# Kernel optimization log

Measured on AMD Instinct MI355X. Metric: run time of the kernel, lower is better.

Reference implementation:

```python
import jax, jax.numpy as jnp
import numpy as np

VOCAB, EMBD, H1, H2, OUT = 100000, 128, 256, 128, 1
EPS = 1e-12

def _layernorm(x, g, b):
    mu = jnp.mean(x, axis=-1, keepdims=True)
    var = jnp.mean(jnp.square(x - mu), axis=-1, keepdims=True)
    return (x - mu) * jax.lax.rsqrt(var + EPS) * g + b

def setup_inputs() -> dict:
    key = jax.random.key(0)
    ks = jax.random.split(key, 10)
    B, S = 4096, 50
    return {
        "entity_ids": jax.random.randint(ks[0], (B, S), 0, VOCAB),
        "entity_length": jax.random.randint(ks[1], (B,), 0, S + 1),
        "emb_table": jax.random.normal(ks[2], (VOCAB, EMBD), jnp.float32),
        "ln1_g": jnp.ones((EMBD,), jnp.float32),
        "ln1_b": jnp.zeros((EMBD,), jnp.float32),
        "w1": jax.random.normal(ks[3], (EMBD, H1), jnp.float32) * (1.0 / np.sqrt(EMBD)),
        "b1": jnp.zeros((H1,), jnp.float32),
        "w2": jax.random.normal(ks[4], (H1, H2), jnp.float32) * (1.0 / np.sqrt(H1)),
        "b2": jnp.zeros((H2,), jnp.float32),
        "ln2_g": jnp.ones((H2,), jnp.float32),
        "ln2_b": jnp.zeros((H2,), jnp.float32),
        "fc_w": jax.random.normal(ks[5], (H2, OUT), jnp.float32) * (1.0 / np.sqrt(H2)),
        "fc_b": jnp.zeros((OUT,), jnp.float32),
    }

def reference(entity_ids, entity_length, emb_table, ln1_g, ln1_b, w1, b1, w2, b2, ln2_g, ln2_b, fc_w, fc_b):
    # embed: [B, S, EMBD]
    x = emb_table[entity_ids]
    x = _layernorm(x, ln1_g, ln1_b)
    # MLP (dropout is identity in eval); torch GELU default is exact erf form
    x = jax.nn.gelu(x @ w1 + b1, approximate=False) @ w2 + b2  # [B, S, H2]
    # ragged max-pool over first length positions (length 0 treated as 1)
    lengths = jnp.maximum(entity_length, 1)  # [B]
    S = x.shape[1]
    mask = jnp.arange(S)[None, :] < lengths[:, None]  # [B, S]
    x = jnp.max(jnp.where(mask[:, :, None], x, -jnp.inf), axis=1)  # [B, H2]
    x = _layernorm(x, ln2_g, ln2_b)
    return (x @ fc_w + fc_b).squeeze(-1)  # [B]
```

## Files before the change

### kernel.cpp

```cpp
#include <hip/hip_runtime.h>
#include <hip/hip_bf16.h>
#include <math.h>

typedef __attribute__((ext_vector_type(8))) short short8;
typedef __attribute__((ext_vector_type(4))) float f32x4;

#define EMBD 128
#define H1 256
#define H2 128
#define SLEN 50

__device__ __forceinline__ short f2bf(float f) {
    __hip_bfloat16 h = __float2bfloat16(f);
    return *reinterpret_cast<short*>(&h);
}

__device__ __forceinline__ float gelu_exact(float h) {
    float ah = fabsf(h);
    float d  = fmaf(0.23163845f, ah, 1.0f);
    float t;
    asm("v_rcp_f32 %0, %1" : "=v"(t) : "v"(d));
    float p = fmaf(1.061405429f, t, -1.453152027f);
    p = fmaf(p, t, 1.421413741f);
    p = fmaf(p, t, -0.284496736f);
    p = fmaf(p, t, 0.254829592f);
    p = p * t;
    float e;
    float x2 = h * h * -0.72134752f;
    asm("v_exp_f32 %0, %1" : "=v"(e) : "v"(x2));
    float er = fmaf(-p, e, 1.0f);
    return fmaf(0.5f * ah, er, 0.5f * h);
}

#define BARRIER_LDS() asm volatile("s_waitcnt lgkmcnt(0)\n\ts_barrier" ::: "memory")

__global__ __launch_bounds__(256) void prep_weights(
    const float* __restrict__ w1, const float* __restrict__ w2,
    short8* __restrict__ ws)
{
    int f = blockIdx.x * 256 + threadIdx.x;
    short8 v;
    if (f < 4096) {
        int lane = f & 63;
        int nt = (f >> 6) & 3, kt = (f >> 8) & 3, w = (f >> 10) & 3;
        int col = w * 64 + nt * 16 + (lane & 15);
        int kb  = kt * 32 + (lane >> 4) * 8;
        #pragma unroll
        for (int i = 0; i < 8; ++i) v[i] = f2bf(w1[(size_t)(kb + i) * H1 + col]);
        ws[f] = v;
    } else {
        int f2 = f - 4096;
        int lane = f2 & 63;
        int nt = (f2 >> 6) & 1, kt = (f2 >> 7) & 7, w = (f2 >> 10) & 3;
        int col = w * 32 + nt * 16 + (lane & 15);
        int kb  = kt * 32 + (lane >> 4) * 8;
        #pragma unroll
        for (int i = 0; i < 8; ++i) v[i] = f2bf(w2[(size_t)(kb + i) * H2 + col]);
        ws[4096 + f2] = v;
    }
}

__global__ __launch_bounds__(256) void entity_encoder_kernel(
    const int* __restrict__ ids, const int* __restrict__ lens,
    const float* __restrict__ emb, const float* __restrict__ ln1g,
    const float* __restrict__ ln1b, const float* __restrict__ b1,
    const float* __restrict__ b2, const float* __restrict__ ln2g,
    const float* __restrict__ ln2b, const float* __restrict__ fcw,
    const float* __restrict__ fcb, const short8* __restrict__ wfrag,
    float* __restrict__ out)
{
    const int tid = threadIdx.x;
    const int w  = tid >> 6;
    const int l  = tid & 63;
    const int ln = l & 15;
    const int lg = l >> 4;

    __shared__ __align__(16) short x_lds[16][EMBD + 8];
    __shared__ __align__(16) short h1_lds[16][H1 + 8];
    __shared__ float pool_lds[H2];

    short8 w1f[4][4];
    #pragma unroll
    for (int kt = 0; kt < 4; ++kt)
      #pragma unroll
      for (int nt = 0; nt < 4; ++nt)
        w1f[kt][nt] = wfrag[((w * 4 + kt) * 4 + nt) * 64 + l];
    short8 w2f[8][2];
    #pragma unroll
    for (int kt = 0; kt < 8; ++kt)
      #pragma unroll
      for (int nt = 0; nt < 2; ++nt)
        w2f[kt][nt] = wfrag[4096 + ((w * 8 + kt) * 2 + nt) * 64 + l];

    float g1r[8], b1r[8];
    #pragma unroll
    for (int i = 0; i < 8; ++i) { g1r[i] = ln1g[ln * 8 + i]; b1r[i] = ln1b[ln * 8 + i]; }
    float b1v[4];
    #pragma unroll
    for (int nt = 0; nt < 4; ++nt) b1v[nt] = b1[w * 64 + nt * 16 + ln];
    float b2v[2];
    #pragma unroll
    for (int nt = 0; nt < 2; ++nt) b2v[nt] = b2[w * 32 + nt * 16 + ln];
    float g2a = ln2g[l], g2c = ln2g[l + 64];
    float b2a = ln2b[l], b2c = ln2b[l + 64];
    float fwa = fcw[l],  fwc = fcw[l + 64];
    float fcb0 = fcb[0];

    const int r = blockIdx.x;
    int T = lens[r]; T = T < 1 ? 1 : (T > SLEN ? SLEN : T);
    const int ntiles = (T + 15) >> 4;
    float pool0 = -INFINITY, pool1 = -INFINITY;

    const int tok = w * 4 + lg;

    float4 pa0, pa1; bool va;
    {
        int t = tok; va = (t < T);
        if (va) {
            int id = ids[r * SLEN + t];
            const float4* src = (const float4*)(emb + (size_t)id * EMBD + ln * 8);
            pa0 = src[0]; pa1 = src[1];
        }
    }

    for (int mt = 0; mt < ntiles; ++mt) {
        short8 xo;
        if (va) {
            float v[8] = {pa0.x, pa0.y, pa0.z, pa0.w, pa1.x, pa1.y, pa1.z, pa1.w};
            float s = 0.f, ss = 0.f;
            #pragma unroll
            for (int i = 0; i < 8; ++i) { s += v[i]; ss += v[i] * v[i]; }
            #pragma unroll
            for (int m = 1; m < 16; m <<= 1) {
                s  += __shfl_xor(s,  m, 64);
                ss += __shfl_xor(ss, m, 64);
            }
            float mu  = s * (1.f / 128.f);
            float var = ss * (1.f / 128.f) - mu * mu;
            float rs  = rsqrtf(var + 1e-12f);
            #pragma unroll
            for (int i = 0; i < 8; ++i)
                xo[i] = f2bf((v[i] - mu) * rs * g1r[i] + b1r[i]);
        } else {
            #pragma unroll
            for (int i = 0; i < 8; ++i) xo[i] = 0;
        }
        *(short8*)&x_lds[tok][ln * 8] = xo;

        float4 pb0, pb1; bool vb = false;
        {
            int tn = (mt + 1) * 16 + tok;
            if (mt + 1 < ntiles && tn < T) {
                vb = true;
                int id = ids[r * SLEN + tn];
                const float4* src = (const float4*)(emb + (size_t)id * EMBD + ln * 8);
                pb0 = src[0]; pb1 = src[1];
            }
        }

        BARRIER_LDS();

        f32x4 acc[4] = {{0,0,0,0},{0,0,0,0},{0,0,0,0},{0,0,0,0}};
        #pragma unroll
        for (int kt = 0; kt < 4; ++kt) {
            short8 a = *(const short8*)&x_lds[ln][kt * 32 + lg * 8];
            #pragma unroll
            for (int nt = 0; nt < 4; ++nt)
                acc[nt] = __builtin_amdgcn_mfma_f32_16x16x32_bf16(a, w1f[kt][nt], acc[nt], 0, 0, 0);
        }
        #pragma unroll
        for (int nt = 0; nt < 4; ++nt) {
            int col = w * 64 + nt * 16 + ln;
            #pragma unroll
            for (int g2 = 0; g2 < 4; ++g2) {
                int row = lg * 4 + g2;
                float h = acc[nt][g2] + b1v[nt];
                h1_lds[row][col] = f2bf(gelu_exact(h));
            }
        }

        BARRIER_LDS();

        f32x4 acc2[2] = {{0,0,0,0},{0,0,0,0}};
        #pragma unroll
        for (int kt = 0; kt < 8; ++kt) {
            short8 a = *(const short8*)&h1_lds[ln][kt * 32 + lg * 8];
            #pragma unroll
            for (int nt = 0; nt < 2; ++nt)
                acc2[nt] = __builtin_amdgcn_mfma_f32_16x16x32_bf16(a, w2f[kt][nt], acc2[nt], 0, 0, 0);
        }
        {
            float tm0 = -INFINITY, tm1 = -INFINITY;
            #pragma unroll
            for (int g2 = 0; g2 < 4; ++g2) {
                int trow = lg * 4 + g2;
                bool valid = (mt * 16 + trow) < T;
                float h0  = acc2[0][g2] + b2v[0];
                float h1v = acc2[1][g2] + b2v[1];
                if (valid) { tm0 = fmaxf(tm0, h0); tm1 = fmaxf(tm1, h1v); }
            }
            tm0 = fmaxf(tm0, __shfl_xor(tm0, 16, 64));
            tm0 = fmaxf(tm0, __shfl_xor(tm0, 32, 64));
            tm1 = fmaxf(tm1, __shfl_xor(tm1, 16, 64));
            tm1 = fmaxf(tm1, __shfl_xor(tm1, 32, 64));
            pool0 = fmaxf(pool0, tm0);
            pool1 = fmaxf(pool1, tm1);
        }

        if (vb) { pa0 = pb0; pa1 = pb1; }
        va = vb;
    }

    if (l < 16) {
        pool_lds[w * 32 + ln]      = pool0;
        pool_lds[w * 32 + 16 + ln] = pool1;
    }
    __syncthreads();

    float v0 = pool_lds[l], v1 = pool_lds[l + 64];
    float s = v0 + v1, ss = v0 * v0 + v1 * v1;
    #pragma unroll
    for (int m = 1; m < 64; m <<= 1) {
        s  += __shfl_xor(s,  m, 64);
        ss += __shfl_xor(ss, m, 64);
    }
    float mu  = s * (1.f / 128.f);
    float var = ss * (1.f / 128.f) - mu * mu;
    float rs  = rsqrtf(var + 1e-12f);
    float n0 = (v0 - mu) * rs * g2a + b2a;
    float n1 = (v1 - mu) * rs * g2c + b2c;
    float dot = n0 * fwa + n1 * fwc;
    #pragma unroll
    for (int m = 1; m < 64; m <<= 1) dot += __shfl_xor(dot, m, 64);
    if (tid == 0) out[r] = dot + fcb0;
}

extern "C" void kernel_launch(void* const* d_in, const int* in_sizes, int n_in,
                              void* d_out, int out_size, void* d_ws, size_t ws_size,
                              hipStream_t stream) {
    const int*   ids  = (const int*)d_in[0];
    const int*   lens = (const int*)d_in[1];
    const float* emb  = (const float*)d_in[2];
    const float* ln1g = (const float*)d_in[3];
    const float* ln1b = (const float*)d_in[4];
    const float* w1   = (const float*)d_in[5];
    const float* b1   = (const float*)d_in[6];
    const float* w2   = (const float*)d_in[7];
    const float* b2   = (const float*)d_in[8];
    const float* ln2g = (const float*)d_in[9];
    const float* ln2b = (const float*)d_in[10];
    const float* fcw  = (const float*)d_in[11];
    const float* fcb  = (const float*)d_in[12];
    float* out = (float*)d_out;
    short8* ws = (short8*)d_ws;

    hipLaunchKernelGGL(prep_weights, dim3(32), dim3(256), 0, stream, w1, w2, ws);

    int nblocks = out_size;
    hipLaunchKernelGGL(entity_encoder_kernel, dim3(nblocks), dim3(256), 0, stream,
                       ids, lens, emb, ln1g, ln1b, b1, b2, ln2g, ln2b, fcw, fcb,
                       ws, out);
}
```

Measured before the change: 74.53 us.

## Process four batch rows per block to amortize weight fragment loads

Each block now handles NR=4 batch rows, strided by grid size, instead of one. The per-block setup of loading W1/W2 MFMA fragments and LayerNorm parameters into registers is paid once per four rows. The embedding prefetch now carries across row boundaries. The cost is a quarter as many blocks (1024 on a 4096 batch), which cuts parallelism and latency hiding. Ragged lengths also make per-block work less even.

```diff
diff --git a/kernel.cpp b/kernel.cpp
--- a/kernel.cpp
+++ b/kernel.cpp
@@ -9,6 +9,7 @@
 #define H1 256
 #define H2 128
 #define SLEN 50
+#define NR 4
 
 __device__ __forceinline__ short f2bf(float f) {
     __hip_bfloat16 h = __float2bfloat16(f);
@@ -106,133 +107,150 @@
     float fwa = fcw[l],  fwc = fcw[l + 64];
     float fcb0 = fcb[0];
 
-    const int r = blockIdx.x;
-    int T = lens[r]; T = T < 1 ? 1 : (T > SLEN ? SLEN : T);
-    const int ntiles = (T + 15) >> 4;
-    float pool0 = -INFINITY, pool1 = -INFINITY;
-
+    const int stride = gridDim.x;
     const int tok = w * 4 + lg;
+
+    int rows[NR], Ts[NR];
+    #pragma unroll
+    for (int i = 0; i < NR; ++i) {
+        rows[i] = blockIdx.x + i * stride;
+        int T = lens[rows[i]];
+        Ts[i] = T < 1 ? 1 : (T > SLEN ? SLEN : T);
+    }
 
     float4 pa0, pa1; bool va;
     {
-        int t = tok; va = (t < T);
+        va = (tok < Ts[0]);
         if (va) {
-            int id = ids[r * SLEN + t];
+            int id = ids[rows[0] * SLEN + tok];
             const float4* src = (const float4*)(emb + (size_t)id * EMBD + ln * 8);
             pa0 = src[0]; pa1 = src[1];
         }
     }
 
-    for (int mt = 0; mt < ntiles; ++mt) {
-        short8 xo;
-        if (va) {
-            float v[8] = {pa0.x, pa0.y, pa0.z, pa0.w, pa1.x, pa1.y, pa1.z, pa1.w};
-            float s = 0.f, ss = 0.f;
+    for (int i = 0; i < NR; ++i) {
+        const int r = rows[i];
+        const int T = Ts[i];
+        const int ntiles = (T + 15) >> 4;
+        float pool0 = -INFINITY, pool1 = -INFINITY;
+
+        for (int mt = 0; mt < ntiles; ++mt) {
+            short8 xo;
+            if (va) {
+                float v[8] = {pa0.x, pa0.y, pa0.z, pa0.w, pa1.x, pa1.y, pa1.z, pa1.w};
+                float s = 0.f, ss = 0.f;
+                #pragma unroll
+                for (int k = 0; k < 8; ++k) { s += v[k]; ss += v[k] * v[k]; }
+                #pragma unroll
+                for (int m = 1; m < 16; m <<= 1) {
+                    s  += __shfl_xor(s,  m, 64);
+                    ss += __shfl_xor(ss, m, 64);
+                }
+                float mu  = s * (1.f / 128.f);
+                float var = ss * (1.f / 128.f) - mu * mu;
+                float rs  = rsqrtf(var + 1e-12f);
+                #pragma unroll
+                for (int k = 0; k < 8; ++k)
+                    xo[k] = f2bf((v[k] - mu) * rs * g1r[k] + b1r[k]);
+            } else {
+                #pragma unroll
+                for (int k = 0; k < 8; ++k) xo[k] = 0;
+            }
+            *(short8*)&x_lds[tok][ln * 8] = xo;
+
+            float4 pb0, pb1; bool vb = false;
+            {
+                int ni = i, nmt = mt + 1;
+                if (nmt >= ntiles) { ni = i + 1; nmt = 0; }
+                if (ni < NR) {
+                    int tn = nmt * 16 + tok;
+                    if (tn < Ts[ni]) {
+                        vb = true;
+                        int id = ids[rows[ni] * SLEN + tn];
+                        const float4* src = (const float4*)(emb + (size_t)id * EMBD + ln * 8);
+                        pb0 = src[0]; pb1 = src[1];
+                    }
+                }
+            }
+
+            BARRIER_LDS();
+
+            f32x4 acc[4] = {{0,0,0,0},{0,0,0,0},{0,0,0,0},{0,0,0,0}};
             #pragma unroll
-            for (int i = 0; i < 8; ++i) { s += v[i]; ss += v[i] * v[i]; }
+            for (int kt = 0; kt < 4; ++kt) {
+                short8 a = *(const short8*)&x_lds[ln][kt * 32 + lg * 8];
+                #pragma unroll
+                for (int nt = 0; nt < 4; ++nt)
+                    acc[nt] = __builtin_amdgcn_mfma_f32_16x16x32_bf16(a, w1f[kt][nt], acc[nt], 0, 0, 0);
+            }
             #pragma unroll
-            for (int m = 1; m < 16; m <<= 1) {
-                s  += __shfl_xor(s,  m, 64);
-                ss += __shfl_xor(ss, m, 64);
-            }
-            float mu  = s * (1.f / 128.f);
-            float var = ss * (1.f / 128.f) - mu * mu;
-            float rs  = rsqrtf(var + 1e-12f);
+            for (int nt = 0; nt < 4; ++nt) {
+                int col = w * 64 + nt * 16 + ln;
+                #pragma unroll
+                for (int g2 = 0; g2 < 4; ++g2) {
+                    int row = lg * 4 + g2;
+                    float h = acc[nt][g2] + b1v[nt];
+                    h1_lds[row][col] = f2bf(gelu_exact(h));
+                }
+            }
+
+            BARRIER_LDS();
+
+            f32x4 acc2[2] = {{0,0,0,0},{0,0,0,0}};
             #pragma unroll
-            for (int i = 0; i < 8; ++i)
-                xo[i] = f2bf((v[i] - mu) * rs * g1r[i] + b1r[i]);
-        } else {
-            #pragma unroll
-            for (int i = 0; i < 8; ++i) xo[i] = 0;
-        }
-        *(short8*)&x_lds[tok][ln * 8] = xo;
-
-        float4 pb0, pb1; bool vb = false;
-        {
-            int tn = (mt + 1) * 16 + tok;
-            if (mt + 1 < ntiles && tn < T) {
-                vb = true;
-                int id = ids[r * SLEN + tn];
-                const float4* src = (const float4*)(emb + (size_t)id * EMBD + ln * 8);
-                pb0 = src[0]; pb1 = src[1];
-            }
-        }
-
+            for (int kt = 0; kt < 8; ++kt) {
+                short8 a = *(const short8*)&h1_lds[ln][kt * 32 + lg * 8];
+                #pragma unroll
+                for (int nt = 0; nt < 2; ++nt)
+                    acc2[nt] = __builtin_amdgcn_mfma_f32_16x16x32_bf16(a, w2f[kt][nt], acc2[nt], 0, 0, 0);
+            }
+            {
+                float tm0 = -INFINITY, tm1 = -INFINITY;
+                #pragma unroll
+                for (int g2 = 0; g2 < 4; ++g2) {
+                    int trow = lg * 4 + g2;
+                    bool valid = (mt * 16 + trow) < T;
+                    float h0  = acc2[0][g2] + b2v[0];
+                    float h1v = acc2[1][g2] + b2v[1];
+                    if (valid) { tm0 = fmaxf(tm0, h0); tm1 = fmaxf(tm1, h1v); }
+                }
+                tm0 = fmaxf(tm0, __shfl_xor(tm0, 16, 64));
+                tm0 = fmaxf(tm0, __shfl_xor(tm0, 32, 64));
+                tm1 = fmaxf(tm1, __shfl_xor(tm1, 16, 64));
+                tm1 = fmaxf(tm1, __shfl_xor(tm1, 32, 64));
+                pool0 = fmaxf(pool0, tm0);
+                pool1 = fmaxf(pool1, tm1);
+            }
+
+            if (vb) { pa0 = pb0; pa1 = pb1; }
+            va = vb;
+        }
+
+        if (l < 16) {
+            pool_lds[w * 32 + ln]      = pool0;
+            pool_lds[w * 32 + 16 + ln] = pool1;
+        }
         BARRIER_LDS();
 
-        f32x4 acc[4] = {{0,0,0,0},{0,0,0,0},{0,0,0,0},{0,0,0,0}};
-        #pragma unroll
-        for (int kt = 0; kt < 4; ++kt) {
-            short8 a = *(const short8*)&x_lds[ln][kt * 32 + lg * 8];
-            #pragma unroll
-            for (int nt = 0; nt < 4; ++nt)
-                acc[nt] = __builtin_amdgcn_mfma_f32_16x16x32_bf16(a, w1f[kt][nt], acc[nt], 0, 0, 0);
-        }
-        #pragma unroll
-        for (int nt = 0; nt < 4; ++nt) {
-            int col = w * 64 + nt * 16 + ln;
-            #pragma unroll
-            for (int g2 = 0; g2 < 4; ++g2) {
-                int row = lg * 4 + g2;
-                float h = acc[nt][g2] + b1v[nt];
-                h1_lds[row][col] = f2bf(gelu_exact(h));
-            }
-        }
+        float v0 = pool_lds[l], v1 = pool_lds[l + 64];
+        float s = v0 + v1, ss = v0 * v0 + v1 * v1;
+        #pragma unroll
+        for (int m = 1; m < 64; m <<= 1) {
+            s  += __shfl_xor(s,  m, 64);
+            ss += __shfl_xor(ss, m, 64);
+        }
+        float mu  = s * (1.f / 128.f);
+        float var = ss * (1.f / 128.f) - mu * mu;
+        float rs  = rsqrtf(var + 1e-12f);
+        float n0 = (v0 - mu) * rs * g2a + b2a;
+        float n1 = (v1 - mu) * rs * g2c + b2c;
+        float dot = n0 * fwa + n1 * fwc;
+        #pragma unroll
+        for (int m = 1; m < 64; m <<= 1) dot += __shfl_xor(dot, m, 64);
+        if (tid == 0) out[r] = dot + fcb0;
 
         BARRIER_LDS();
-
-        f32x4 acc2[2] = {{0,0,0,0},{0,0,0,0}};
-        #pragma unroll
-        for (int kt = 0; kt < 8; ++kt) {
-            short8 a = *(const short8*)&h1_lds[ln][kt * 32 + lg * 8];
-            #pragma unroll
-            for (int nt = 0; nt < 2; ++nt)
-                acc2[nt] = __builtin_amdgcn_mfma_f32_16x16x32_bf16(a, w2f[kt][nt], acc2[nt], 0, 0, 0);
-        }
-        {
-            float tm0 = -INFINITY, tm1 = -INFINITY;
-            #pragma unroll
-            for (int g2 = 0; g2 < 4; ++g2) {
-                int trow = lg * 4 + g2;
-                bool valid = (mt * 16 + trow) < T;
-                float h0  = acc2[0][g2] + b2v[0];
-                float h1v = acc2[1][g2] + b2v[1];
-                if (valid) { tm0 = fmaxf(tm0, h0); tm1 = fmaxf(tm1, h1v); }
-            }
-            tm0 = fmaxf(tm0, __shfl_xor(tm0, 16, 64));
-            tm0 = fmaxf(tm0, __shfl_xor(tm0, 32, 64));
-            tm1 = fmaxf(tm1, __shfl_xor(tm1, 16, 64));
-            tm1 = fmaxf(tm1, __shfl_xor(tm1, 32, 64));
-            pool0 = fmaxf(pool0, tm0);
-            pool1 = fmaxf(pool1, tm1);
-        }
-
-        if (vb) { pa0 = pb0; pa1 = pb1; }
-        va = vb;
-    }
-
-    if (l < 16) {
-        pool_lds[w * 32 + ln]      = pool0;
-        pool_lds[w * 32 + 16 + ln] = pool1;
-    }
-    __syncthreads();
-
-    float v0 = pool_lds[l], v1 = pool_lds[l + 64];
-    float s = v0 + v1, ss = v0 * v0 + v1 * v1;
-    #pragma unroll
-    for (int m = 1; m < 64; m <<= 1) {
-        s  += __shfl_xor(s,  m, 64);
-        ss += __shfl_xor(ss, m, 64);
-    }
-    float mu  = s * (1.f / 128.f);
-    float var = ss * (1.f / 128.f) - mu * mu;
-    float rs  = rsqrtf(var + 1e-12f);
-    float n0 = (v0 - mu) * rs * g2a + b2a;
-    float n1 = (v1 - mu) * rs * g2c + b2c;
-    float dot = n0 * fwa + n1 * fwc;
-    #pragma unroll
-    for (int m = 1; m < 64; m <<= 1) dot += __shfl_xor(dot, m, 64);
-    if (tid == 0) out[r] = dot + fcb0;
+    }
 }
 
 extern "C" void kernel_launch(void* const* d_in, const int* in_sizes, int n_in,
@@ -256,7 +274,7 @@
 
     hipLaunchKernelGGL(prep_weights, dim3(32), dim3(256), 0, stream, w1, w2, ws);
 
-    int nblocks = out_size;
+    int nblocks = out_size / NR;
     hipLaunchKernelGGL(entity_encoder_kernel, dim3(nblocks), dim3(256), 0, stream,
                        ids, lens, emb, ln1g, ln1b, b1, b2, ln2g, ln2b, fcw, fcb,
                        ws, out);
```

New measurement: 70.42 us. 5.5% less time.
